# Kernel tuning notes

Hardware: AMD Instinct MI355X
Metric: run time of the kernel (lower is better)

Reference implementation:

```python
import jax, jax.numpy as jnp
from jax import lax
import numpy as np

B, S, D, H2, V = 1024, 256, 128, 5, 50257
EPS = 1e-5


def setup_inputs() -> dict:
    key = jax.random.key(0)
    ks = jax.random.split(key, 12)
    s = 0.08  # init scale ~ 1/sqrt(D)
    return {
        "x": jax.random.randint(ks[0], (B, S), 0, V),
        "emb": jax.random.normal(ks[1], (V, D), jnp.float32) * s,
        "W_ih1": jax.random.normal(ks[2], (D, D), jnp.float32) * s,
        "b_ih1": jax.random.normal(ks[3], (D,), jnp.float32) * s,
        "W_hh1": jax.random.normal(ks[4], (D, D), jnp.float32) * s,
        "b_hh1": jax.random.normal(ks[5], (D,), jnp.float32) * s,
        "g1": jnp.ones((D,), jnp.float32),
        "be1": jnp.zeros((D,), jnp.float32),
        "W_ih2": jax.random.normal(ks[6], (H2, D), jnp.float32) * s,
        "b_ih2": jax.random.normal(ks[7], (H2,), jnp.float32) * s,
        "W_hh2": jax.random.normal(ks[8], (H2, H2), jnp.float32) * s,
        "b_hh2": jax.random.normal(ks[9], (H2,), jnp.float32) * s,
        "g2": jnp.ones((H2,), jnp.float32),
        "be2": jnp.zeros((H2,), jnp.float32),
    }


def _rnn(xproj, W_hh):
    """Vanilla tanh RNN. xproj: [B,S,H] = x @ W_ih^T + b_ih + b_hh (precomputed)."""
    h0 = jnp.zeros((xproj.shape[0], W_hh.shape[0]), xproj.dtype)

    def step(h, xt):  # xt: [B,H]
        h = jnp.tanh(xt + h @ W_hh.T)
        return h, h

    _, hs = lax.scan(step, h0, jnp.swapaxes(xproj, 0, 1))  # [S,B,H]
    return jnp.swapaxes(hs, 0, 1)  # [B,S,H]


def _ln(z, g, b):
    m = jnp.mean(z, axis=-1, keepdims=True)
    v = jnp.mean(jnp.square(z - m), axis=-1, keepdims=True)
    return (z - m) * lax.rsqrt(v + EPS) * g + b


def reference(x, emb, W_ih1, b_ih1, W_hh1, b_hh1, g1, be1,
              W_ih2, b_ih2, W_hh2, b_hh2, g2, be2):
    e = emb[x]  # [B,S,D]
    z = _rnn(e @ W_ih1.T + (b_ih1 + b_hh1), W_hh1)
    z = _ln(z, g1, be1)
    z = _rnn(z @ W_ih2.T + (b_ih2 + b_hh2), W_hh2)  # [B,S,5]
    z = _ln(z, g2, be2)
    pooled = jnp.mean(z, axis=1)  # AvgPool1d over full seq -> [B,5]
    return jax.nn.softmax(pooled, axis=1)
```

## Files before the change

### kernel.cpp

```cpp
#include <hip/hip_runtime.h>
#include <stdint.h>

#define S_LEN 256
#define DIM   128
#define EPSL  1e-5f

typedef __bf16 bf16x8 __attribute__((ext_vector_type(8)));
typedef float  f32x4  __attribute__((ext_vector_type(4)));

__device__ __forceinline__ unsigned short f2bf_bits(float f) {
  union { float f; unsigned int u; } v; v.f = f;
  unsigned int r = v.u + 0x7fffu + ((v.u >> 16) & 1u);
  return (unsigned short)(r >> 16);
}
__device__ __forceinline__ float bf2f_bits(unsigned short b) {
  union { float f; unsigned int u; } v; v.u = ((unsigned int)b) << 16; return v.f;
}
__device__ __forceinline__ unsigned f2bf_rhu(float f) {
  return (__float_as_uint(f) + 0x8000u) >> 16;
}
__device__ __forceinline__ unsigned pack_rhu(float lo, float hi) {
  return __builtin_amdgcn_perm(__float_as_uint(hi) + 0x8000u,
                               __float_as_uint(lo) + 0x8000u, 0x07060302u);
}
__device__ __forceinline__ float tanh_fast(float x) {
  float e = __expf(2.f * x);
  return 1.f - 2.f * __builtin_amdgcn_rcpf(e + 1.f);
}

template<int CTRL>
__device__ __forceinline__ float dpp_rot_add(float v) {
  int r = __builtin_amdgcn_update_dpp(0, __float_as_int(v), CTRL, 0xF, 0xF, true);
  return v + __int_as_float(r);
}
template<int CTRL>
__device__ __forceinline__ float dpp_rot_max(float v) {
  int r = __builtin_amdgcn_update_dpp(0, __float_as_int(v), CTRL, 0xF, 0xF, true);
  return fmaxf(v, __int_as_float(r));
}
__device__ __forceinline__ float dpp_sum16(float v) {
  v = dpp_rot_add<0x124>(v); v = dpp_rot_add<0x128>(v);
  v = dpp_rot_add<0x39>(v);  v = dpp_rot_add<0x4E>(v);
  return v;
}
__device__ __forceinline__ float dpp_max16(float v) {
  v = dpp_rot_max<0x124>(v); v = dpp_rot_max<0x128>(v);
  v = dpp_rot_max<0x39>(v);  v = dpp_rot_max<0x4E>(v);
  return v;
}
template<int CTRL>
__device__ __forceinline__ void red_level7(float& s, float& sq, float* d) {
  s  = dpp_rot_add<CTRL>(s);
  sq = dpp_rot_add<CTRL>(sq);
#pragma unroll
  for (int j = 0; j < 5; j++) d[j] = dpp_rot_add<CTRL>(d[j]);
}
template<int JJ>
__device__ __forceinline__ float bcast16(float v) {
  int r = __builtin_amdgcn_ds_swizzle(__float_as_int(v), (JJ << 5) | 0x10);
  return __int_as_float(r);
}

union Frag8 { unsigned short us[8]; bf16x8 v; int4 i4; };

__global__ __launch_bounds__(512, 2)
void xproj_pre(const int* __restrict__ x, const float* __restrict__ emb,
               const float* __restrict__ Wih1, const float* __restrict__ bih1,
               const float* __restrict__ bhh1, unsigned short* __restrict__ ws)
{
  __shared__ __align__(16) unsigned short e_s[16 * 128];
  const int tid  = threadIdx.x;
  const int wave = tid >> 6;
  const int lane = tid & 63;
  const int l15  = lane & 15;
  const int q    = lane >> 4;
  const int bb   = blockIdx.x >> 4;
  const int tc   = blockIdx.x & 15;
  const int r0   = bb * 16;

  const int n1 = wave * 16 + l15;
  const float bias1v = bih1[n1] + bhh1[n1];
  bf16x8 wih[4];
#pragma unroll
  for (int kt = 0; kt < 4; kt++) {
    int k0 = kt * 32 + q * 8;
    Frag8 fa;
#pragma unroll
    for (int j = 0; j < 8; j++) fa.us[j] = f2bf_bits(Wih1[n1 * DIM + k0 + j]);
    wih[kt] = fa.v;
  }

  for (int tt = 0; tt < 16; tt++) {
    const int t = tc * 16 + tt;
    if (tid < 256) {
      int m = tid >> 4, oct = tid & 15;
      int xid = x[(size_t)(r0 + m) * S_LEN + t];
      const float* pe = emb + (size_t)xid * DIM + oct * 8;
      float4 lv0 = *(const float4*)pe;
      float4 lv1 = *(const float4*)(pe + 4);
      int4 pk;
      pk.x = pack_rhu(lv0.x, lv0.y); pk.y = pack_rhu(lv0.z, lv0.w);
      pk.z = pack_rhu(lv1.x, lv1.y); pk.w = pack_rhu(lv1.z, lv1.w);
      *(int4*)&e_s[m * 128 + ((oct ^ m) & 15) * 8] = pk;
    }
    __syncthreads();
    f32x4 a = {bias1v, bias1v, bias1v, bias1v};
#pragma unroll
    for (int kt = 0; kt < 4; kt++) {
      int sw = (((kt * 4 + q) ^ l15) & 15) * 8;
      bf16x8 ae = *(const bf16x8*)&e_s[l15 * 128 + sw];
      a = __builtin_amdgcn_mfma_f32_16x16x32_bf16(ae, wih[kt], a, 0, 0, 0);
    }
    uint2 st;
    st.x = pack_rhu(a[0], a[1]); st.y = pack_rhu(a[2], a[3]);
    *(uint2*)&ws[(((size_t)t * 64 + bb) * 128 + n1) * 16 + q * 4] = st;
    __syncthreads();
  }
}

__global__ __launch_bounds__(512, 2)
void rnn_serial(const unsigned short* __restrict__ xp,
                const float* __restrict__ Whh1,
                const float* __restrict__ g1,  const float* __restrict__ be1,
                const float* __restrict__ Wih2, const float* __restrict__ bih2,
                const float* __restrict__ Whh2, const float* __restrict__ bhh2,
                const float* __restrict__ g2,  const float* __restrict__ be2,
                float* __restrict__ out)
{
  __shared__ __align__(16) unsigned short h_bf[2][16 * 128];
  const int tid  = threadIdx.x;
  const int wave = tid >> 6;
  const int lane = tid & 63;
  const int bb   = blockIdx.x;
  const int r0   = bb * 16;
  const int l15  = lane & 15;
  const int q    = lane >> 4;

  for (int i = tid; i < 16 * 128; i += 512) h_bf[1][i] = 0;

  const int n1 = wave * 16 + l15;
  bf16x8 whi[4], wlo[4];
#pragma unroll
  for (int kt = 0; kt < 4; kt++) {
    int k0 = kt * 32 + q * 8;
    Frag8 fh, fl;
#pragma unroll
    for (int j = 0; j < 8; j++) {
      float w = Whh1[n1 * DIM + k0 + j];
      unsigned short hi = f2bf_bits(w);
      fh.us[j] = hi;
      fl.us[j] = f2bf_bits(w - bf2f_bits(hi));
    }
    whi[kt] = fh.v; wlo[kt] = fl.v;
  }
  const size_t xofs = ((size_t)bb * 128 + n1) * 16 + q * 4;

  const bool ln_role = (wave < 4);
  float w2g[5][8], Gs[5], Bs[5], wrow[5];
  float t2_l = 0.f, g2_l = 0.f, be2_l = 0.f, validf = 0.f;
  float h2rep[5], pool_l = 0.f;
  int myrow = 0;
  if (ln_role) {
    myrow = wave * 4 + q;
    int coct = (l15 ^ myrow) & 15;
#pragma unroll
    for (int j = 0; j < 8; j++) {
      int c = coct * 8 + j;
      float gc = g1[c];
#pragma unroll
      for (int jj = 0; jj < 5; jj++) w2g[jj][j] = Wih2[jj * DIM + c] * gc;
    }
#pragma unroll
    for (int jj = 0; jj < 5; jj++) { Gs[jj] = 0.f; Bs[jj] = 0.f; }
    for (int c = 0; c < DIM; c++) {
      float gc = g1[c], bc = be1[c];
#pragma unroll
      for (int jj = 0; jj < 5; jj++) {
        float w = Wih2[jj * DIM + c];
        Gs[jj] += w * gc; Bs[jj] += w * bc;
      }
    }
    validf = (l15 < 5) ? 1.f : 0.f;
    if (l15 < 5) {
      t2_l = bih2[l15] + bhh2[l15];
      g2_l = g2[l15]; be2_l = be2[l15];
#pragma unroll
      for (int jj = 0; jj < 5; jj++) wrow[jj] = Whh2[l15 * 5 + jj];
    } else {
#pragma unroll
      for (int jj = 0; jj < 5; jj++) wrow[jj] = 0.f;
    }
#pragma unroll
    for (int jj = 0; jj < 5; jj++) h2rep[jj] = 0.f;
  }

  uint2 pfx[2];
  pfx[0] = *(const uint2*)&xp[xofs];
  pfx[1] = *(const uint2*)&xp[xofs + 131072];
  __syncthreads();

#pragma unroll 2
  for (int t = 0; t <= S_LEN; t++) {
    if (t < S_LEN) {
      uint2 cur = pfx[t & 1];
      if (t + 2 < S_LEN)
        pfx[t & 1] = *(const uint2*)&xp[xofs + (size_t)(t + 2) * 131072];
      const int rb = (t + 1) & 1;
      f32x4 ah = {0.f, 0.f, 0.f, 0.f}, al = {0.f, 0.f, 0.f, 0.f};
#pragma unroll
      for (int kt = 0; kt < 4; kt++) {
        int sw = (((kt * 4 + q) ^ l15) & 15) * 8;
        bf16x8 ahf = *(const bf16x8*)&h_bf[rb][l15 * 128 + sw];
        ah = __builtin_amdgcn_mfma_f32_16x16x32_bf16(ahf, whi[kt], ah, 0, 0, 0);
        al = __builtin_amdgcn_mfma_f32_16x16x32_bf16(ahf, wlo[kt], al, 0, 0, 0);
      }
      float xq[4];
      xq[0] = __uint_as_float(cur.x << 16);
      xq[1] = __uint_as_float(cur.x & 0xffff0000u);
      xq[2] = __uint_as_float(cur.y << 16);
      xq[3] = __uint_as_float(cur.y & 0xffff0000u);
      const int wb = t & 1;
      const int c = n1;
      const int oct = c >> 3;
#pragma unroll
      for (int r = 0; r < 4; r++) {
        int row = q * 4 + r;
        float av = ah[r] + al[r] + xq[r];
        h_bf[wb][row * 128 + ((oct ^ row) & 15) * 8 + (c & 7)] =
            (unsigned short)f2bf_rhu(tanh_fast(av));
      }
    }
    if (ln_role && t >= 1) {
      const int hb = (t - 1) & 1;
      Frag8 hr;
      hr.i4 = *(const int4*)&h_bf[hb][myrow * 128 + l15 * 8];
      float s = 0.f, sq = 0.f, d[5] = {0, 0, 0, 0, 0};
#pragma unroll
      for (int j = 0; j < 8; j++) {
        float v = bf2f_bits(hr.us[j]);
        s += v; sq += v * v;
#pragma unroll
        for (int jj = 0; jj < 5; jj++) d[jj] = fmaf(w2g[jj][j], v, d[jj]);
      }
      red_level7<0x124>(s, sq, d);
      red_level7<0x128>(s, sq, d);
      red_level7<0x39>(s, sq, d);
      red_level7<0x4E>(s, sq, d);
      float mean = s * (1.f / 128.f);
      float var  = sq * (1.f / 128.f) - mean * mean;
      float rstd = rsqrtf(var + EPSL);
      float p[5];
#pragma unroll
      for (int jj = 0; jj < 5; jj++)
        p[jj] = rstd * (d[jj] - mean * Gs[jj]) + Bs[jj];
      float psel = (l15 == 0) ? p[0] : (l15 == 1) ? p[1] :
                   (l15 == 2) ? p[2] : (l15 == 3) ? p[3] : p[4];
      float a = psel + t2_l;
#pragma unroll
      for (int jj = 0; jj < 5; jj++) a = fmaf(wrow[jj], h2rep[jj], a);
      float xn = tanh_fast(a);
      h2rep[0] = bcast16<0>(xn); h2rep[1] = bcast16<1>(xn);
      h2rep[2] = bcast16<2>(xn); h2rep[3] = bcast16<3>(xn);
      h2rep[4] = bcast16<4>(xn);
      float s2 = dpp_sum16(xn * validf) * 0.2f;
      float dd = xn - s2;
      float v2 = dpp_sum16(dd * dd * validf) * 0.2f;
      float r2 = rsqrtf(v2 + EPSL);
      pool_l += dd * r2 * g2_l + be2_l;
    }
    asm volatile("s_waitcnt lgkmcnt(0)\n\ts_barrier" ::: "memory");
  }

  if (ln_role) {
    float lg = pool_l * (1.f / 256.f);
    float mx = dpp_max16((l15 < 5) ? lg : -3.0e38f);
    float e  = (l15 < 5) ? __expf(lg - mx) : 0.f;
    float sm = dpp_sum16(e);
    if (l15 < 5) out[(size_t)(r0 + myrow) * 5 + l15] = e / sm;
  }
}

__global__ __launch_bounds__(512, 2)
void rnn_fused_fb(const int* __restrict__ x, const float* __restrict__ emb,
                  const float* __restrict__ Wih1, const float* __restrict__ bih1,
                  const float* __restrict__ Whh1, const float* __restrict__ bhh1,
                  const float* __restrict__ g1, const float* __restrict__ be1,
                  const float* __restrict__ Wih2, const float* __restrict__ bih2,
                  const float* __restrict__ Whh2, const float* __restrict__ bhh2,
                  const float* __restrict__ g2, const float* __restrict__ be2,
                  float* __restrict__ out)
{
  __shared__ __align__(16) unsigned short h_bf[2][16 * 128];
  __shared__ __align__(16) unsigned short e_bf[2][16 * 128];
  __shared__ int x_tile[16 * 256];

  const int tid  = threadIdx.x;
  const int wave = tid >> 6;
  const int lane = tid & 63;
  const int r0   = blockIdx.x * 16;
  const int l15  = lane & 15;
  const int q    = lane >> 4;

  for (int i = tid; i < 16 * 256; i += 512)
    x_tile[i] = x[(size_t)(r0 + (i >> 8)) * S_LEN + (i & 255)];
  for (int i = tid; i < 16 * 128; i += 512) h_bf[1][i] = 0;

  const int n1 = wave * 16 + l15;
  const float bias1v = bih1[n1] + bhh1[n1];
  bf16x8 whi[4], wlo[4], wih[4];
#pragma unroll
  for (int kt = 0; kt < 4; kt++) {
    int k0 = kt * 32 + q * 8;
    Frag8 fh, fl, fa;
#pragma unroll
    for (int j = 0; j < 8; j++) {
      float w = Whh1[n1 * DIM + k0 + j];
      unsigned short hi = f2bf_bits(w);
      fh.us[j] = hi;
      fl.us[j] = f2bf_bits(w - bf2f_bits(hi));
      fa.us[j] = f2bf_bits(Wih1[n1 * DIM + k0 + j]);
    }
    whi[kt] = fh.v; wlo[kt] = fl.v; wih[kt] = fa.v;
  }

  const bool ln_role = (wave < 4);
  float w2g[5][8], Gs[5], Bs[5], wrow[5];
  float t2_l = 0.f, g2_l = 0.f, be2_l = 0.f, validf = 0.f;
  float h2rep[5], pool_l = 0.f;
  int myrow = 0;
  float pf[2][8];
  const int gm   = (wave & 3) * 4 + q;
  const int goct = l15;
  const int gdst = gm * 128 + ((goct ^ gm) & 15) * 8;

  if (ln_role) {
    myrow = wave * 4 + q;
    int coct = (l15 ^ myrow) & 15;
#pragma unroll
    for (int j = 0; j < 8; j++) {
      int c = coct * 8 + j;
      float gc = g1[c];
#pragma unroll
      for (int jj = 0; jj < 5; jj++) w2g[jj][j] = Wih2[jj * DIM + c] * gc;
    }
#pragma unroll
    for (int jj = 0; jj < 5; jj++) { Gs[jj] = 0.f; Bs[jj] = 0.f; }
    for (int c = 0; c < DIM; c++) {
      float gc = g1[c], bc = be1[c];
#pragma unroll
      for (int jj = 0; jj < 5; jj++) {
        float w = Wih2[jj * DIM + c];
        Gs[jj] += w * gc; Bs[jj] += w * bc;
      }
    }
    validf = (l15 < 5) ? 1.f : 0.f;
    if (l15 < 5) {
      t2_l = bih2[l15] + bhh2[l15];
      g2_l = g2[l15]; be2_l = be2[l15];
#pragma unroll
      for (int jj = 0; jj < 5; jj++) wrow[jj] = Whh2[l15 * 5 + jj];
    } else {
#pragma unroll
      for (int jj = 0; jj < 5; jj++) wrow[jj] = 0.f;
    }
#pragma unroll
    for (int jj = 0; jj < 5; jj++) h2rep[jj] = 0.f;
  }
  __syncthreads();

  if (!ln_role) {
    float ta[8], tb[8];
    { int xid = x_tile[gm * 256 + 0];
      const float* pe = emb + (size_t)xid * DIM + goct * 8;
#pragma unroll
      for (int j = 0; j < 8; j++) ta[j] = pe[j]; }
    { int xid = x_tile[gm * 256 + 1];
      const float* pe = emb + (size_t)xid * DIM + goct * 8;
#pragma unroll
      for (int j = 0; j < 8; j++) tb[j] = pe[j]; }
    { int xid = x_tile[gm * 256 + 2];
      const float* pe = emb + (size_t)xid * DIM + goct * 8;
#pragma unroll
      for (int j = 0; j < 8; j++) pf[0][j] = pe[j]; }
    { int xid = x_tile[gm * 256 + 3];
      const float* pe = emb + (size_t)xid * DIM + goct * 8;
#pragma unroll
      for (int j = 0; j < 8; j++) pf[1][j] = pe[j]; }
    Frag8 pa, pb;
#pragma unroll
    for (int j = 0; j < 8; j++) { pa.us[j] = f2bf_bits(ta[j]); pb.us[j] = f2bf_bits(tb[j]); }
    *(int4*)&e_bf[0][gdst] = pa.i4;
    *(int4*)&e_bf[1][gdst] = pb.i4;
  }
  __syncthreads();

  f32x4 xpacc = {bias1v, bias1v, bias1v, bias1v};
#pragma unroll
  for (int kt = 0; kt < 4; kt++) {
    int sw = (((kt * 4 + q) ^ l15) & 15) * 8;
    bf16x8 ae = *(const bf16x8*)&e_bf[0][l15 * 128 + sw];
    xpacc = __builtin_amdgcn_mfma_f32_16x16x32_bf16(ae, wih[kt], xpacc, 0, 0, 0);
  }
  asm volatile("s_waitcnt lgkmcnt(0)\n\ts_barrier" ::: "memory");

#pragma unroll 2
  for (int t = 0; t <= S_LEN; t++) {
    f32x4 ah = {0.f, 0.f, 0.f, 0.f};
    f32x4 al = xpacc;
    if (t < S_LEN) {
      const int rb = (t + 1) & 1;
#pragma unroll
      for (int kt = 0; kt < 4; kt++) {
        int sw = (((kt * 4 + q) ^ l15) & 15) * 8;
        bf16x8 ahf = *(const bf16x8*)&h_bf[rb][l15 * 128 + sw];
        ah = __builtin_amdgcn_mfma_f32_16x16x32_bf16(ahf, whi[kt], ah, 0, 0, 0);
        al = __builtin_amdgcn_mfma_f32_16x16x32_bf16(ahf, wlo[kt], al, 0, 0, 0);
      }
    }
    if (t + 1 < S_LEN) {
      f32x4 a = {bias1v, bias1v, bias1v, bias1v};
#pragma unroll
      for (int kt = 0; kt < 4; kt++) {
        int sw = (((kt * 4 + q) ^ l15) & 15) * 8;
        bf16x8 ae = *(const bf16x8*)&e_bf[(t + 1) & 1][l15 * 128 + sw];
        a = __builtin_amdgcn_mfma_f32_16x16x32_bf16(ae, wih[kt], a, 0, 0, 0);
      }
      xpacc = a;
    }
    if (t < S_LEN) {
      const int wb = t & 1;
      const int c = wave * 16 + l15;
      const int oct = c >> 3;
#pragma unroll
      for (int r = 0; r < 4; r++) {
        int row = q * 4 + r;
        float av = ah[r] + al[r];
        h_bf[wb][row * 128 + ((oct ^ row) & 15) * 8 + (c & 7)] =
            (unsigned short)f2bf_rhu(tanh_fast(av));
      }
    }
    if (!ln_role) {
      if (t + 2 < S_LEN) {
        int4 pk;
        pk.x = pack_rhu(pf[t & 1][0], pf[t & 1][1]);
        pk.y = pack_rhu(pf[t & 1][2], pf[t & 1][3]);
        pk.z = pack_rhu(pf[t & 1][4], pf[t & 1][5]);
        pk.w = pack_rhu(pf[t & 1][6], pf[t & 1][7]);
        *(int4*)&e_bf[t & 1][gdst] = pk;
      }
      if (t + 4 < S_LEN) {
        int xid = x_tile[gm * 256 + t + 4];
        const float* pe = emb + (size_t)xid * DIM + goct * 8;
#pragma unroll
        for (int j = 0; j < 8; j++) pf[t & 1][j] = pe[j];
      }
    } else if (t >= 1) {
      const int hb = (t - 1) & 1;
      Frag8 hr;
      hr.i4 = *(const int4*)&h_bf[hb][myrow * 128 + l15 * 8];
      float s = 0.f, sq = 0.f, d[5] = {0, 0, 0, 0, 0};
#pragma unroll
      for (int j = 0; j < 8; j++) {
        float v = bf2f_bits(hr.us[j]);
        s += v; sq += v * v;
#pragma unroll
        for (int jj = 0; jj < 5; jj++) d[jj] = fmaf(w2g[jj][j], v, d[jj]);
      }
      red_level7<0x124>(s, sq, d);
      red_level7<0x128>(s, sq, d);
      red_level7<0x39>(s, sq, d);
      red_level7<0x4E>(s, sq, d);
      float mean = s * (1.f / 128.f);
      float var  = sq * (1.f / 128.f) - mean * mean;
      float rstd = rsqrtf(var + EPSL);
      float p[5];
#pragma unroll
      for (int jj = 0; jj < 5; jj++)
        p[jj] = rstd * (d[jj] - mean * Gs[jj]) + Bs[jj];
      float psel = (l15 == 0) ? p[0] : (l15 == 1) ? p[1] :
                   (l15 == 2) ? p[2] : (l15 == 3) ? p[3] : p[4];
      float a = psel + t2_l;
#pragma unroll
      for (int jj = 0; jj < 5; jj++) a = fmaf(wrow[jj], h2rep[jj], a);
      float xn = tanh_fast(a);
      h2rep[0] = bcast16<0>(xn); h2rep[1] = bcast16<1>(xn);
      h2rep[2] = bcast16<2>(xn); h2rep[3] = bcast16<3>(xn);
      h2rep[4] = bcast16<4>(xn);
      float s2 = dpp_sum16(xn * validf) * 0.2f;
      float dd = xn - s2;
      float v2 = dpp_sum16(dd * dd * validf) * 0.2f;
      float r2 = rsqrtf(v2 + EPSL);
      pool_l += dd * r2 * g2_l + be2_l;
    }
    asm volatile("s_waitcnt lgkmcnt(0)\n\ts_barrier" ::: "memory");
  }

  if (ln_role) {
    float lg = pool_l * (1.f / 256.f);
    float mx = dpp_max16((l15 < 5) ? lg : -3.0e38f);
    float e  = (l15 < 5) ? __expf(lg - mx) : 0.f;
    float sm = dpp_sum16(e);
    if (l15 < 5) out[(size_t)(r0 + myrow) * 5 + l15] = e / sm;
  }
}

extern "C" void kernel_launch(void* const* d_in, const int* in_sizes, int n_in,
                              void* d_out, int out_size, void* d_ws, size_t ws_size,
                              hipStream_t stream) {
  (void)in_sizes; (void)n_in; (void)out_size;
  const int*   x    = (const int*)  d_in[0];
  const float* emb  = (const float*)d_in[1];
  const float* Wih1 = (const float*)d_in[2];
  const float* bih1 = (const float*)d_in[3];
  const float* Whh1 = (const float*)d_in[4];
  const float* bhh1 = (const float*)d_in[5];
  const float* g1   = (const float*)d_in[6];
  const float* be1  = (const float*)d_in[7];
  const float* Wih2 = (const float*)d_in[8];
  const float* bih2 = (const float*)d_in[9];
  const float* Whh2 = (const float*)d_in[10];
  const float* bhh2 = (const float*)d_in[11];
  const float* g2   = (const float*)d_in[12];
  const float* be2  = (const float*)d_in[13];
  float* out = (float*)d_out;

  const size_t XPBYTES = (size_t)S_LEN * 64 * 128 * 16 * 2;
  if (ws_size >= XPBYTES) {
    unsigned short* ws = (unsigned short*)d_ws;
    xproj_pre<<<dim3(1024), dim3(512), 0, stream>>>(x, emb, Wih1, bih1, bhh1, ws);
    rnn_serial<<<dim3(64), dim3(512), 0, stream>>>(ws, Whh1, g1, be1, Wih2,
                                                   bih2, Whh2, bhh2, g2, be2, out);
  } else {
    rnn_fused_fb<<<dim3(64), dim3(512), 0, stream>>>(
        x, emb, Wih1, bih1, Whh1, bhh1, g1, be1,
        Wih2, bih2, Whh2, bhh2, g2, be2, out);
  }
}
```

Before: 319.3 us.

## Split RNN into layer-1 core kernel and separate layer-2 tail kernel

Restructures the pipeline. The layer-1 recurrence now computes the input projection in-kernel from staged embeddings and writes every hidden state to workspace. A second kernel runs LayerNorm, the 5-wide second RNN and the pooling with many more blocks. This removes the separate xproj pass and its workspace round trip, and takes the per-step layer-2 work off the serial critical path. It also drops the hi/lo split of W_hh1 to a single bf16 MFMA chain, which halves the recurrent MFMAs but lowers precision. The cost is writing and re-reading a 64MB hidden-state buffer.

```diff
diff --git a/kernel.cpp b/kernel.cpp
--- a/kernel.cpp
+++ b/kernel.cpp
@@ -64,220 +64,245 @@
 union Frag8 { unsigned short us[8]; bf16x8 v; int4 i4; };
 
 __global__ __launch_bounds__(512, 2)
-void xproj_pre(const int* __restrict__ x, const float* __restrict__ emb,
-               const float* __restrict__ Wih1, const float* __restrict__ bih1,
-               const float* __restrict__ bhh1, unsigned short* __restrict__ ws)
+void rnn_core(const int* __restrict__ x, const float* __restrict__ emb,
+              const float* __restrict__ Wih1, const float* __restrict__ bih1,
+              const float* __restrict__ Whh1, const float* __restrict__ bhh1,
+              unsigned short* __restrict__ hout)
 {
-  __shared__ __align__(16) unsigned short e_s[16 * 128];
+  __shared__ __align__(16) unsigned short h_bf[2][16 * 128];
+  __shared__ __align__(16) unsigned short e_bf[2][16 * 128];
+  __shared__ int x_tile[16 * 256];
+
+  const int tid  = threadIdx.x;
+  const int wave = tid >> 6;
+  const int lane = tid & 63;
+  const int r0   = blockIdx.x * 16;
+  const int l15  = lane & 15;
+  const int q    = lane >> 4;
+
+  for (int i = tid; i < 16 * 256; i += 512)
+    x_tile[i] = x[(size_t)(r0 + (i >> 8)) * S_LEN + (i & 255)];
+  for (int i = tid; i < 16 * 128; i += 512) h_bf[1][i] = 0;
+
+  const int n1 = wave * 16 + l15;
+  const float bias1v = bih1[n1] + bhh1[n1];
+  bf16x8 wh[4], wih[4];
+#pragma unroll
+  for (int kt = 0; kt < 4; kt++) {
+    int k0 = kt * 32 + q * 8;
+    Frag8 fh, fa;
+#pragma unroll
+    for (int j = 0; j < 8; j++) {
+      fh.us[j] = f2bf_bits(Whh1[n1 * DIM + k0 + j]);
+      fa.us[j] = f2bf_bits(Wih1[n1 * DIM + k0 + j]);
+    }
+    wh[kt] = fh.v; wih[kt] = fa.v;
+  }
+
+  const bool stage_role = (wave >= 4);
+  float pf[2][8];
+  const int gm   = (wave & 3) * 4 + q;
+  const int goct = l15;
+  const int gdst = gm * 128 + ((goct ^ gm) & 15) * 8;
+  __syncthreads();
+
+  if (stage_role) {
+    float ta[8], tb[8];
+    { int xid = x_tile[gm * 256 + 0];
+      const float* pe = emb + (size_t)xid * DIM + goct * 8;
+#pragma unroll
+      for (int j = 0; j < 8; j++) ta[j] = pe[j]; }
+    { int xid = x_tile[gm * 256 + 1];
+      const float* pe = emb + (size_t)xid * DIM + goct * 8;
+#pragma unroll
+      for (int j = 0; j < 8; j++) tb[j] = pe[j]; }
+    { int xid = x_tile[gm * 256 + 2];
+      const float* pe = emb + (size_t)xid * DIM + goct * 8;
+#pragma unroll
+      for (int j = 0; j < 8; j++) pf[0][j] = pe[j]; }
+    { int xid = x_tile[gm * 256 + 3];
+      const float* pe = emb + (size_t)xid * DIM + goct * 8;
+#pragma unroll
+      for (int j = 0; j < 8; j++) pf[1][j] = pe[j]; }
+    Frag8 pa, pb;
+#pragma unroll
+    for (int j = 0; j < 8; j++) { pa.us[j] = f2bf_bits(ta[j]); pb.us[j] = f2bf_bits(tb[j]); }
+    *(int4*)&e_bf[0][gdst] = pa.i4;
+    *(int4*)&e_bf[1][gdst] = pb.i4;
+  }
+  __syncthreads();
+
+  f32x4 xpacc = {bias1v, bias1v, bias1v, bias1v};
+#pragma unroll
+  for (int kt = 0; kt < 4; kt++) {
+    int sw = (((kt * 4 + q) ^ l15) & 15) * 8;
+    bf16x8 ae = *(const bf16x8*)&e_bf[0][l15 * 128 + sw];
+    xpacc = __builtin_amdgcn_mfma_f32_16x16x32_bf16(ae, wih[kt], xpacc, 0, 0, 0);
+  }
+  asm volatile("s_waitcnt lgkmcnt(0)\n\ts_barrier" ::: "memory");
+
+#pragma unroll 2
+  for (int t = 0; t < S_LEN; t++) {
+    f32x4 acc = xpacc;
+    {
+      const int rb = (t + 1) & 1;
+#pragma unroll
+      for (int kt = 0; kt < 4; kt++) {
+        int sw = (((kt * 4 + q) ^ l15) & 15) * 8;
+        bf16x8 ahf = *(const bf16x8*)&h_bf[rb][l15 * 128 + sw];
+        acc = __builtin_amdgcn_mfma_f32_16x16x32_bf16(ahf, wh[kt], acc, 0, 0, 0);
+      }
+      const int wb = t & 1;
+      const int oct = n1 >> 3;
+#pragma unroll
+      for (int r = 0; r < 4; r++) {
+        int row = q * 4 + r;
+        unsigned short us = (unsigned short)f2bf_rhu(tanh_fast(acc[r]));
+        h_bf[wb][row * 128 + ((oct ^ row) & 15) * 8 + (n1 & 7)] = us;
+        hout[((size_t)(r0 + row) * S_LEN + t) * DIM + n1] = us;
+      }
+    }
+
+    if (t + 1 < S_LEN) {
+      f32x4 a = {bias1v, bias1v, bias1v, bias1v};
+#pragma unroll
+      for (int kt = 0; kt < 4; kt++) {
+        int sw = (((kt * 4 + q) ^ l15) & 15) * 8;
+        bf16x8 ae = *(const bf16x8*)&e_bf[(t + 1) & 1][l15 * 128 + sw];
+        a = __builtin_amdgcn_mfma_f32_16x16x32_bf16(ae, wih[kt], a, 0, 0, 0);
+      }
+      xpacc = a;
+    }
+
+    if (stage_role) {
+      if (t + 2 < S_LEN) {
+        int4 pk;
+        pk.x = pack_rhu(pf[t & 1][0], pf[t & 1][1]);
+        pk.y = pack_rhu(pf[t & 1][2], pf[t & 1][3]);
+        pk.z = pack_rhu(pf[t & 1][4], pf[t & 1][5]);
+        pk.w = pack_rhu(pf[t & 1][6], pf[t & 1][7]);
+        *(int4*)&e_bf[t & 1][gdst] = pk;
+      }
+      if (t + 4 < S_LEN) {
+        int xid = x_tile[gm * 256 + t + 4];
+        const float* pe = emb + (size_t)xid * DIM + goct * 8;
+#pragma unroll
+        for (int j = 0; j < 8; j++) pf[t & 1][j] = pe[j];
+      }
+    }
+    asm volatile("s_waitcnt lgkmcnt(0)\n\ts_barrier" ::: "memory");
+  }
+}
+
+__global__ __launch_bounds__(256, 2)
+void rnn_tail(const unsigned short* __restrict__ hall,
+              const float* __restrict__ g1,  const float* __restrict__ be1,
+              const float* __restrict__ Wih2, const float* __restrict__ bih2,
+              const float* __restrict__ Whh2, const float* __restrict__ bhh2,
+              const float* __restrict__ g2,  const float* __restrict__ be2,
+              float* __restrict__ out)
+{
+  __shared__ float p_lds[4][4][8];
   const int tid  = threadIdx.x;
   const int wave = tid >> 6;
   const int lane = tid & 63;
   const int l15  = lane & 15;
   const int q    = lane >> 4;
-  const int bb   = blockIdx.x >> 4;
-  const int tc   = blockIdx.x & 15;
-  const int r0   = bb * 16;
-
-  const int n1 = wave * 16 + l15;
-  const float bias1v = bih1[n1] + bhh1[n1];
-  bf16x8 wih[4];
-#pragma unroll
-  for (int kt = 0; kt < 4; kt++) {
-    int k0 = kt * 32 + q * 8;
-    Frag8 fa;
-#pragma unroll
-    for (int j = 0; j < 8; j++) fa.us[j] = f2bf_bits(Wih1[n1 * DIM + k0 + j]);
-    wih[kt] = fa.v;
-  }
-
-  for (int tt = 0; tt < 16; tt++) {
-    const int t = tc * 16 + tt;
-    if (tid < 256) {
-      int m = tid >> 4, oct = tid & 15;
-      int xid = x[(size_t)(r0 + m) * S_LEN + t];
-      const float* pe = emb + (size_t)xid * DIM + oct * 8;
-      float4 lv0 = *(const float4*)pe;
-      float4 lv1 = *(const float4*)(pe + 4);
-      int4 pk;
-      pk.x = pack_rhu(lv0.x, lv0.y); pk.y = pack_rhu(lv0.z, lv0.w);
-      pk.z = pack_rhu(lv1.x, lv1.y); pk.w = pack_rhu(lv1.z, lv1.w);
-      *(int4*)&e_s[m * 128 + ((oct ^ m) & 15) * 8] = pk;
-    }
-    __syncthreads();
-    f32x4 a = {bias1v, bias1v, bias1v, bias1v};
-#pragma unroll
-    for (int kt = 0; kt < 4; kt++) {
-      int sw = (((kt * 4 + q) ^ l15) & 15) * 8;
-      bf16x8 ae = *(const bf16x8*)&e_s[l15 * 128 + sw];
-      a = __builtin_amdgcn_mfma_f32_16x16x32_bf16(ae, wih[kt], a, 0, 0, 0);
-    }
-    uint2 st;
-    st.x = pack_rhu(a[0], a[1]); st.y = pack_rhu(a[2], a[3]);
-    *(uint2*)&ws[(((size_t)t * 64 + bb) * 128 + n1) * 16 + q * 4] = st;
-    __syncthreads();
-  }
-}
-
-__global__ __launch_bounds__(512, 2)
-void rnn_serial(const unsigned short* __restrict__ xp,
-                const float* __restrict__ Whh1,
-                const float* __restrict__ g1,  const float* __restrict__ be1,
-                const float* __restrict__ Wih2, const float* __restrict__ bih2,
-                const float* __restrict__ Whh2, const float* __restrict__ bhh2,
-                const float* __restrict__ g2,  const float* __restrict__ be2,
-                float* __restrict__ out)
-{
-  __shared__ __align__(16) unsigned short h_bf[2][16 * 128];
-  const int tid  = threadIdx.x;
-  const int wave = tid >> 6;
-  const int lane = tid & 63;
-  const int bb   = blockIdx.x;
-  const int r0   = bb * 16;
-  const int l15  = lane & 15;
-  const int q    = lane >> 4;
-
-  for (int i = tid; i < 16 * 128; i += 512) h_bf[1][i] = 0;
-
-  const int n1 = wave * 16 + l15;
-  bf16x8 whi[4], wlo[4];
-#pragma unroll
-  for (int kt = 0; kt < 4; kt++) {
-    int k0 = kt * 32 + q * 8;
-    Frag8 fh, fl;
+  const int b    = blockIdx.x * 4 + wave;
+
+  float w2g[5][8], Gs[5], Bs[5], wrow[5];
+#pragma unroll
+  for (int j = 0; j < 8; j++) {
+    int c = l15 * 8 + j;
+    float gc = g1[c];
+#pragma unroll
+    for (int jj = 0; jj < 5; jj++) w2g[jj][j] = Wih2[jj * DIM + c] * gc;
+  }
+#pragma unroll
+  for (int jj = 0; jj < 5; jj++) { Gs[jj] = 0.f; Bs[jj] = 0.f; }
+  for (int c = 0; c < DIM; c++) {
+    float gc = g1[c], bc = be1[c];
+#pragma unroll
+    for (int jj = 0; jj < 5; jj++) {
+      float w = Wih2[jj * DIM + c];
+      Gs[jj] += w * gc; Bs[jj] += w * bc;
+    }
+  }
+  const float validf = (l15 < 5) ? 1.f : 0.f;
+  float t2_l = 0.f, g2_l = 0.f, be2_l = 0.f;
+  if (l15 < 5) {
+    t2_l = bih2[l15] + bhh2[l15];
+    g2_l = g2[l15]; be2_l = be2[l15];
+#pragma unroll
+    for (int jj = 0; jj < 5; jj++) wrow[jj] = Whh2[l15 * 5 + jj];
+  } else {
+#pragma unroll
+    for (int jj = 0; jj < 5; jj++) wrow[jj] = 0.f;
+  }
+  float h2rep[5];
+#pragma unroll
+  for (int jj = 0; jj < 5; jj++) h2rep[jj] = 0.f;
+  float pool_l = 0.f;
+
+  const unsigned short* hb = hall + (size_t)b * S_LEN * DIM;
+  uint4 hpre = *(const uint4*)(hb + q * DIM + l15 * 8);
+
+  for (int t0 = 0; t0 < S_LEN; t0 += 4) {
+    uint4 cur = hpre;
+    if (t0 + 4 < S_LEN)
+      hpre = *(const uint4*)(hb + (size_t)(t0 + 4 + q) * DIM + l15 * 8);
+    float hv[8];
+    hv[0] = __uint_as_float(cur.x << 16); hv[1] = __uint_as_float(cur.x & 0xffff0000u);
+    hv[2] = __uint_as_float(cur.y << 16); hv[3] = __uint_as_float(cur.y & 0xffff0000u);
+    hv[4] = __uint_as_float(cur.z << 16); hv[5] = __uint_as_float(cur.z & 0xffff0000u);
+    hv[6] = __uint_as_float(cur.w << 16); hv[7] = __uint_as_float(cur.w & 0xffff0000u);
+    float s = 0.f, sq = 0.f, d[5] = {0, 0, 0, 0, 0};
 #pragma unroll
     for (int j = 0; j < 8; j++) {
-      float w = Whh1[n1 * DIM + k0 + j];
-      unsigned short hi = f2bf_bits(w);
-      fh.us[j] = hi;
-      fl.us[j] = f2bf_bits(w - bf2f_bits(hi));
-    }
-    whi[kt] = fh.v; wlo[kt] = fl.v;
-  }
-  const size_t xofs = ((size_t)bb * 128 + n1) * 16 + q * 4;
-
-  const bool ln_role = (wave < 4);
-  float w2g[5][8], Gs[5], Bs[5], wrow[5];
-  float t2_l = 0.f, g2_l = 0.f, be2_l = 0.f, validf = 0.f;
-  float h2rep[5], pool_l = 0.f;
-  int myrow = 0;
-  if (ln_role) {
-    myrow = wave * 4 + q;
-    int coct = (l15 ^ myrow) & 15;
-#pragma unroll
-    for (int j = 0; j < 8; j++) {
-      int c = coct * 8 + j;
-      float gc = g1[c];
-#pragma unroll
-      for (int jj = 0; jj < 5; jj++) w2g[jj][j] = Wih2[jj * DIM + c] * gc;
-    }
-#pragma unroll
-    for (int jj = 0; jj < 5; jj++) { Gs[jj] = 0.f; Bs[jj] = 0.f; }
-    for (int c = 0; c < DIM; c++) {
-      float gc = g1[c], bc = be1[c];
-#pragma unroll
-      for (int jj = 0; jj < 5; jj++) {
-        float w = Wih2[jj * DIM + c];
-        Gs[jj] += w * gc; Bs[jj] += w * bc;
-      }
-    }
-    validf = (l15 < 5) ? 1.f : 0.f;
-    if (l15 < 5) {
-      t2_l = bih2[l15] + bhh2[l15];
-      g2_l = g2[l15]; be2_l = be2[l15];
-#pragma unroll
-      for (int jj = 0; jj < 5; jj++) wrow[jj] = Whh2[l15 * 5 + jj];
-    } else {
-#pragma unroll
-      for (int jj = 0; jj < 5; jj++) wrow[jj] = 0.f;
-    }
-#pragma unroll
-    for (int jj = 0; jj < 5; jj++) h2rep[jj] = 0.f;
-  }
-
-  uint2 pfx[2];
-  pfx[0] = *(const uint2*)&xp[xofs];
-  pfx[1] = *(const uint2*)&xp[xofs + 131072];
-  __syncthreads();
-
-#pragma unroll 2
-  for (int t = 0; t <= S_LEN; t++) {
-    if (t < S_LEN) {
-      uint2 cur = pfx[t & 1];
-      if (t + 2 < S_LEN)
-        pfx[t & 1] = *(const uint2*)&xp[xofs + (size_t)(t + 2) * 131072];
-      const int rb = (t + 1) & 1;
-      f32x4 ah = {0.f, 0.f, 0.f, 0.f}, al = {0.f, 0.f, 0.f, 0.f};
-#pragma unroll
-      for (int kt = 0; kt < 4; kt++) {
-        int sw = (((kt * 4 + q) ^ l15) & 15) * 8;
-        bf16x8 ahf = *(const bf16x8*)&h_bf[rb][l15 * 128 + sw];
-        ah = __builtin_amdgcn_mfma_f32_16x16x32_bf16(ahf, whi[kt], ah, 0, 0, 0);
-        al = __builtin_amdgcn_mfma_f32_16x16x32_bf16(ahf, wlo[kt], al, 0, 0, 0);
-      }
-      float xq[4];
-      xq[0] = __uint_as_float(cur.x << 16);
-      xq[1] = __uint_as_float(cur.x & 0xffff0000u);
-      xq[2] = __uint_as_float(cur.y << 16);
-      xq[3] = __uint_as_float(cur.y & 0xffff0000u);
-      const int wb = t & 1;
-      const int c = n1;
-      const int oct = c >> 3;
-#pragma unroll
-      for (int r = 0; r < 4; r++) {
-        int row = q * 4 + r;
-        float av = ah[r] + al[r] + xq[r];
-        h_bf[wb][row * 128 + ((oct ^ row) & 15) * 8 + (c & 7)] =
-            (unsigned short)f2bf_rhu(tanh_fast(av));
-      }
-    }
-    if (ln_role && t >= 1) {
-      const int hb = (t - 1) & 1;
-      Frag8 hr;
-      hr.i4 = *(const int4*)&h_bf[hb][myrow * 128 + l15 * 8];
-      float s = 0.f, sq = 0.f, d[5] = {0, 0, 0, 0, 0};
-#pragma unroll
-      for (int j = 0; j < 8; j++) {
-        float v = bf2f_bits(hr.us[j]);
-        s += v; sq += v * v;
-#pragma unroll
-        for (int jj = 0; jj < 5; jj++) d[jj] = fmaf(w2g[jj][j], v, d[jj]);
-      }
-      red_level7<0x124>(s, sq, d);
-      red_level7<0x128>(s, sq, d);
-      red_level7<0x39>(s, sq, d);
-      red_level7<0x4E>(s, sq, d);
-      float mean = s * (1.f / 128.f);
-      float var  = sq * (1.f / 128.f) - mean * mean;
-      float rstd = rsqrtf(var + EPSL);
-      float p[5];
-#pragma unroll
-      for (int jj = 0; jj < 5; jj++)
-        p[jj] = rstd * (d[jj] - mean * Gs[jj]) + Bs[jj];
-      float psel = (l15 == 0) ? p[0] : (l15 == 1) ? p[1] :
-                   (l15 == 2) ? p[2] : (l15 == 3) ? p[3] : p[4];
-      float a = psel + t2_l;
+      float v = hv[j];
+      s += v; sq += v * v;
+#pragma unroll
+      for (int jj = 0; jj < 5; jj++) d[jj] = fmaf(w2g[jj][j], v, d[jj]);
+    }
+    red_level7<0x124>(s, sq, d);
+    red_level7<0x128>(s, sq, d);
+    red_level7<0x39>(s, sq, d);
+    red_level7<0x4E>(s, sq, d);
+    float mean = s * (1.f / 128.f);
+    float var  = sq * (1.f / 128.f) - mean * mean;
+    float rstd = rsqrtf(var + EPSL);
+    float p[5];
+#pragma unroll
+    for (int jj = 0; jj < 5; jj++)
+      p[jj] = rstd * (d[jj] - mean * Gs[jj]) + Bs[jj];
+    float psel = (l15 == 0) ? p[0] : (l15 == 1) ? p[1] :
+                 (l15 == 2) ? p[2] : (l15 == 3) ? p[3] : p[4];
+    if (l15 < 5) p_lds[wave][q][l15] = psel;
+    asm volatile("s_waitcnt lgkmcnt(0)" ::: "memory");
+    const int idx = (l15 < 5) ? l15 : 0;
+#pragma unroll
+    for (int g = 0; g < 4; g++) {
+      float pv = p_lds[wave][g][idx];
+      float a = pv + t2_l;
 #pragma unroll
       for (int jj = 0; jj < 5; jj++) a = fmaf(wrow[jj], h2rep[jj], a);
       float xn = tanh_fast(a);
-      h2rep[0] = bcast16<0>(xn); h2rep[1] = bcast16<1>(xn);
-      h2rep[2] = bcast16<2>(xn); h2rep[3] = bcast16<3>(xn);
-      h2rep[4] = bcast16<4>(xn);
       float s2 = dpp_sum16(xn * validf) * 0.2f;
       float dd = xn - s2;
       float v2 = dpp_sum16(dd * dd * validf) * 0.2f;
       float r2 = rsqrtf(v2 + EPSL);
       pool_l += dd * r2 * g2_l + be2_l;
-    }
-    asm volatile("s_waitcnt lgkmcnt(0)\n\ts_barrier" ::: "memory");
-  }
-
-  if (ln_role) {
-    float lg = pool_l * (1.f / 256.f);
-    float mx = dpp_max16((l15 < 5) ? lg : -3.0e38f);
-    float e  = (l15 < 5) ? __expf(lg - mx) : 0.f;
-    float sm = dpp_sum16(e);
-    if (l15 < 5) out[(size_t)(r0 + myrow) * 5 + l15] = e / sm;
-  }
+      h2rep[0] = bcast16<0>(xn); h2rep[1] = bcast16<1>(xn);
+      h2rep[2] = bcast16<2>(xn); h2rep[3] = bcast16<3>(xn);
+      h2rep[4] = bcast16<4>(xn);
+    }
+  }
+
+  float lg = pool_l * (1.f / 256.f);
+  float mx = dpp_max16((l15 < 5) ? lg : -3.0e38f);
+  float e  = (l15 < 5) ? __expf(lg - mx) : 0.f;
+  float sm = dpp_sum16(e);
+  if (q == 0 && l15 < 5) out[(size_t)b * 5 + l15] = e / sm;
 }
 
 __global__ __launch_bounds__(512, 2)
@@ -307,20 +332,17 @@
 
   const int n1 = wave * 16 + l15;
   const float bias1v = bih1[n1] + bhh1[n1];
-  bf16x8 whi[4], wlo[4], wih[4];
+  bf16x8 wh[4], wih[4];
 #pragma unroll
   for (int kt = 0; kt < 4; kt++) {
     int k0 = kt * 32 + q * 8;
-    Frag8 fh, fl, fa;
+    Frag8 fh, fa;
 #pragma unroll
     for (int j = 0; j < 8; j++) {
-      float w = Whh1[n1 * DIM + k0 + j];
-      unsigned short hi = f2bf_bits(w);
-      fh.us[j] = hi;
-      fl.us[j] = f2bf_bits(w - bf2f_bits(hi));
+      fh.us[j] = f2bf_bits(Whh1[n1 * DIM + k0 + j]);
       fa.us[j] = f2bf_bits(Wih1[n1 * DIM + k0 + j]);
     }
-    whi[kt] = fh.v; wlo[kt] = fl.v; wih[kt] = fa.v;
+    wh[kt] = fh.v; wih[kt] = fa.v;
   }
 
   const bool ln_role = (wave < 4);
@@ -405,16 +427,22 @@
 
 #pragma unroll 2
   for (int t = 0; t <= S_LEN; t++) {
-    f32x4 ah = {0.f, 0.f, 0.f, 0.f};
-    f32x4 al = xpacc;
+    f32x4 acc = xpacc;
     if (t < S_LEN) {
       const int rb = (t + 1) & 1;
 #pragma unroll
       for (int kt = 0; kt < 4; kt++) {
         int sw = (((kt * 4 + q) ^ l15) & 15) * 8;
         bf16x8 ahf = *(const bf16x8*)&h_bf[rb][l15 * 128 + sw];
-        ah = __builtin_amdgcn_mfma_f32_16x16x32_bf16(ahf, whi[kt], ah, 0, 0, 0);
-        al = __builtin_amdgcn_mfma_f32_16x16x32_bf16(ahf, wlo[kt], al, 0, 0, 0);
+        acc = __builtin_amdgcn_mfma_f32_16x16x32_bf16(ahf, wh[kt], acc, 0, 0, 0);
+      }
+      const int wb = t & 1;
+      const int oct = n1 >> 3;
+#pragma unroll
+      for (int r = 0; r < 4; r++) {
+        int row = q * 4 + r;
+        h_bf[wb][row * 128 + ((oct ^ row) & 15) * 8 + (n1 & 7)] =
+            (unsigned short)f2bf_rhu(tanh_fast(acc[r]));
       }
     }
     if (t + 1 < S_LEN) {
@@ -426,18 +454,6 @@
         a = __builtin_amdgcn_mfma_f32_16x16x32_bf16(ae, wih[kt], a, 0, 0, 0);
       }
       xpacc = a;
-    }
-    if (t < S_LEN) {
-      const int wb = t & 1;
-      const int c = wave * 16 + l15;
-      const int oct = c >> 3;
-#pragma unroll
-      for (int r = 0; r < 4; r++) {
-        int row = q * 4 + r;
-        float av = ah[r] + al[r];
-        h_bf[wb][row * 128 + ((oct ^ row) & 15) * 8 + (c & 7)] =
-            (unsigned short)f2bf_rhu(tanh_fast(av));
-      }
     }
     if (!ln_role) {
       if (t + 2 < S_LEN) {
@@ -483,14 +499,14 @@
 #pragma unroll
       for (int jj = 0; jj < 5; jj++) a = fmaf(wrow[jj], h2rep[jj], a);
       float xn = tanh_fast(a);
-      h2rep[0] = bcast16<0>(xn); h2rep[1] = bcast16<1>(xn);
-      h2rep[2] = bcast16<2>(xn); h2rep[3] = bcast16<3>(xn);
-      h2rep[4] = bcast16<4>(xn);
       float s2 = dpp_sum16(xn * validf) * 0.2f;
       float dd = xn - s2;
       float v2 = dpp_sum16(dd * dd * validf) * 0.2f;
       float r2 = rsqrtf(v2 + EPSL);
       pool_l += dd * r2 * g2_l + be2_l;
+      h2rep[0] = bcast16<0>(xn); h2rep[1] = bcast16<1>(xn);
+      h2rep[2] = bcast16<2>(xn); h2rep[3] = bcast16<3>(xn);
+      h2rep[4] = bcast16<4>(xn);
     }
     asm volatile("s_waitcnt lgkmcnt(0)\n\ts_barrier" ::: "memory");
   }
@@ -524,12 +540,12 @@
   const float* be2  = (const float*)d_in[13];
   float* out = (float*)d_out;
 
-  const size_t XPBYTES = (size_t)S_LEN * 64 * 128 * 16 * 2;
-  if (ws_size >= XPBYTES) {
-    unsigned short* ws = (unsigned short*)d_ws;
-    xproj_pre<<<dim3(1024), dim3(512), 0, stream>>>(x, emb, Wih1, bih1, bhh1, ws);
-    rnn_serial<<<dim3(64), dim3(512), 0, stream>>>(ws, Whh1, g1, be1, Wih2,
-                                                   bih2, Whh2, bhh2, g2, be2, out);
+  const size_t HBYTES = (size_t)1024 * S_LEN * DIM * 2;
+  if (ws_size >= HBYTES) {
+    unsigned short* hws = (unsigned short*)d_ws;
+    rnn_core<<<dim3(64), dim3(512), 0, stream>>>(x, emb, Wih1, bih1, Whh1, bhh1, hws);
+    rnn_tail<<<dim3(256), dim3(256), 0, stream>>>(hws, g1, be1, Wih2, bih2,
+                                                  Whh2, bhh2, g2, be2, out);
   } else {
     rnn_fused_fb<<<dim3(64), dim3(512), 0, stream>>>(
         x, emb, Wih1, bih1, Whh1, bhh1, g1, be1,
```

Result: faster. 275.2 us (-13.8%).
